# Performance work log

Measured on AMD Instinct MI355X. Metric: run time of the kernel, lower is better.

Reference implementation:

```python
import jax, jax.numpy as jnp
import numpy as np

N_OBJ = 4096     # number of tree nodes (objects)
IN_DIM = 1024    # inputs_dim (visual feature per node)
EMB = 200        # GloVe embed_dim
HID = 1024       # hidden_dim
NCLS = 151       # len(classes)
IN_SIZE = IN_DIM + EMB  # backward direction: inputs_dim + embed_dim


def _linear_params(k, fan_in, fan_out):
    kw, kb = jax.random.split(k)
    s = 1.0 / np.sqrt(fan_in)
    W = jax.random.uniform(kw, (fan_out, fan_in), jnp.float32, -s, s)
    b = jax.random.uniform(kb, (fan_out,), jnp.float32, -s, s)
    return W, b


def setup_inputs() -> dict:
    key = jax.random.key(0)
    ks = jax.random.split(key, 8)
    features = jax.random.normal(ks[0], (N_OBJ, IN_DIM), jnp.float32)
    embed_W = jax.random.normal(ks[1], (NCLS + 1, EMB), jnp.float32)  # row 0 = 'start'
    W_px, b_px = _linear_params(ks[2], IN_SIZE, HID)
    W_ioux, b_ioux = _linear_params(ks[3], IN_SIZE, 3 * HID)
    W_iouh, b_iouh = _linear_params(ks[4], HID, 3 * HID)
    W_fx, b_fx = _linear_params(ks[5], IN_SIZE, HID)
    W_fh, b_fh = _linear_params(ks[6], HID, HID)
    W_out, b_out = _linear_params(ks[7], HID, NCLS)
    # Irregular random tree in preorder: parent step index always < own step index.
    rng = np.random.RandomState(0)
    parent_pos = np.floor(rng.rand(N_OBJ) * np.arange(N_OBJ)).astype(np.int32)
    parent_pos[0] = -1  # root
    proc_order = rng.permutation(N_OBJ).astype(np.int32)  # node index visited at step t
    return dict(features=features, embed_W=embed_W,
                W_px=W_px, b_px=b_px, W_ioux=W_ioux, b_ioux=b_ioux,
                W_iouh=W_iouh, b_iouh=b_iouh, W_fx=W_fx, b_fx=b_fx,
                W_fh=W_fh, b_fh=b_fh, W_out=W_out, b_out=b_out,
                proc_order=jnp.asarray(proc_order), parent_pos=jnp.asarray(parent_pos),
                num_obj=N_OBJ)


def reference(features, embed_W, W_px, b_px, W_ioux, b_ioux, W_iouh, b_iouh,
              W_fx, b_fx, W_fh, b_fh, W_out, b_out, proc_order, parent_pos, num_obj):
    N = features.shape[0]
    H = W_fh.shape[0]

    def step(carry, t):
        h_all, c_all, lab_all = carry  # states/labels indexed by visit step
        pid = parent_pos[t]
        is_root = pid < 0
        pidc = jnp.maximum(pid, 0)
        ph = jnp.where(is_root, 0.0, h_all[pidc])  # parent hidden (root -> zeros)
        pc = jnp.where(is_root, 0.0, c_all[pidc])  # parent cell
        # input embedding: parent's predicted label (+1 for 'start' offset), root uses 'start' (row 0)
        eidx = jnp.where(is_root, 0, lab_all[pidc] + 1)
        feat = jnp.concatenate([features[proc_order[t]], embed_W[eidx]])  # [IN_SIZE]
        # tree-LSTM cell (node_backward)
        projected_x = W_px @ feat + b_px
        iou = W_ioux @ feat + b_ioux + W_iouh @ ph + b_iouh
        i, o, u = jnp.split(iou, 3)
        i = jax.nn.sigmoid(i); o = jax.nn.sigmoid(o); u = jnp.tanh(u)
        f = jax.nn.sigmoid(W_fx @ feat + b_fx + W_fh @ ph + b_fh)
        c = i * u + f * pc
        h = o * jnp.tanh(c) * jax.nn.sigmoid(projected_x)  # highway-style gate
        dist = W_out @ h + b_out  # [NCLS]
        label = (jnp.argmax(dist[1:]) + 1).astype(jnp.int32)  # skip background, eval-mode argmax
        return (h_all.at[t].set(h), c_all.at[t].set(c), lab_all.at[t].set(label)), (dist, label)

    init = (jnp.zeros((N, H), features.dtype),
            jnp.zeros((N, H), features.dtype),
            jnp.zeros((N,), jnp.int32))
    _, (dists, labels) = jax.lax.scan(step, init, jnp.arange(N))
    # scatter back from visit order to node order (out[node] = value at its visit step)
    out_dists = jnp.zeros_like(dists).at[proc_order].set(dists)
    out_commitments = jnp.zeros((N,), jnp.int32).at[proc_order].set(labels)
    return out_dists, out_commitments
```

## Files before the change

kernel.cpp:

```cpp
#include <hip/hip_runtime.h>
#include <hip/hip_bf16.h>
#include <math.h>

#define N_OBJ 4096
#define IN_DIM 1024
#define EMB_D 200
#define HID 1024
#define NCLS 151
#define IN_SZ 1224
#define NEMB 152
#define R5 5120
#define RH 4096
#define MAXLVL 32

typedef __attribute__((ext_vector_type(8))) short bf16x8;
typedef __attribute__((ext_vector_type(4))) float f32x4;

__device__ __forceinline__ float sigf(float x) { return 1.f / (1.f + expf(-x)); }

__device__ __forceinline__ void split2(float x, ushort& hi, ushort& lo) {
    unsigned u = __float_as_uint(x);
    unsigned r = u + 0x7FFFu + ((u >> 16) & 1u);
    hi = (ushort)(r >> 16);
    float rem = x - __uint_as_float(r & 0xFFFF0000u);
    unsigned u2 = __float_as_uint(rem);
    unsigned r2 = u2 + 0x7FFFu + ((u2 >> 16) & 1u);
    lo = (ushort)(r2 >> 16);
}

__device__ __forceinline__ void gload16(const ushort* src, ushort* dst) {
    __builtin_amdgcn_global_load_lds(
        (const __attribute__((address_space(1))) void*)src,
        (__attribute__((address_space(3))) void*)dst, 16, 0, 0);
}

__global__ __launch_bounds__(1024)
void build_levels(const int* __restrict__ parent_pos,
                  int* __restrict__ level_nodes,
                  int* __restrict__ level_start,
                  ushort* __restrict__ zpad)
{
    __shared__ int dep[N_OBJ];
    __shared__ int par[N_OBJ];
    __shared__ int cnt[MAXLVL];
    __shared__ int offs[MAXLVL];
    __shared__ int base[MAXLVL + 1];
    __shared__ int done;
    const int tid = threadIdx.x;

    if (tid < 1024) zpad[tid] = 0;

    for (int t = tid; t < N_OBJ; t += 1024) {
        int p = parent_pos[t];
        par[t] = p;
        dep[t] = (p < 0) ? 0 : -1;
    }
    for (int l = tid; l < MAXLVL; l += 1024) { cnt[l] = 0; offs[l] = 0; }
    __syncthreads();

    for (int it = 0; it < 64; ++it) {
        if (tid == 0) done = 1;
        __syncthreads();
        for (int t = tid; t < N_OBJ; t += 1024) {
            if (dep[t] < 0) {
                int dp = dep[par[t]];
                if (dp >= 0) dep[t] = dp + 1;
                else done = 0;
            }
        }
        __syncthreads();
        int d = done;
        __syncthreads();
        if (d) break;
    }

    for (int t = tid; t < N_OBJ; t += 1024) {
        int d = dep[t];
        if (d < 0 || d >= MAXLVL) d = MAXLVL - 1;
        dep[t] = d;
        atomicAdd(&cnt[d], 1);
    }
    __syncthreads();
    if (tid == 0) {
        base[0] = 0;
        for (int l = 0; l < MAXLVL; ++l) base[l + 1] = base[l] + cnt[l];
    }
    __syncthreads();
    for (int t = tid; t < N_OBJ; t += 1024) {
        int d = dep[t];
        int pos = base[d] + atomicAdd(&offs[d], 1);
        level_nodes[pos] = t;
    }
    for (int l = tid; l <= MAXLVL; l += 1024) level_start[l] = base[l];
}

__global__ __launch_bounds__(256)
void xemb_kernel(const float* __restrict__ embed_W,
                 const float* __restrict__ W_px,
                 const float* __restrict__ W_ioux,
                 const float* __restrict__ W_fx,
                 const float* __restrict__ b_px,
                 const float* __restrict__ b_ioux,
                 const float* __restrict__ b_iouh,
                 const float* __restrict__ b_fx,
                 const float* __restrict__ b_fh,
                 float* __restrict__ Xemb)
{
    __shared__ float e_s[EMB_D];
    const int e = blockIdx.x;
    const int r = blockIdx.y * 256 + threadIdx.x;
    for (int k = threadIdx.x; k < EMB_D; k += 256) e_s[k] = embed_W[(size_t)e * EMB_D + k];
    __syncthreads();

    const float* wrow;
    float bias;
    if (r < HID) {
        wrow = W_px + (size_t)r * IN_SZ;
        bias = b_px[r];
    } else if (r < 4 * HID) {
        wrow = W_ioux + (size_t)(r - HID) * IN_SZ;
        bias = b_ioux[r - HID] + b_iouh[r - HID];
    } else {
        wrow = W_fx + (size_t)(r - 4 * HID) * IN_SZ;
        bias = b_fx[r - 4 * HID] + b_fh[r - 4 * HID];
    }

    float s = bias;
    for (int k = 0; k < EMB_D; ++k) s += wrow[IN_DIM + k] * e_s[k];
    Xemb[(size_t)e * R5 + r] = s;
}

__global__ __launch_bounds__(256)
void convert_wh(const float* __restrict__ W_iouh, const float* __restrict__ W_fh,
                ushort* __restrict__ Whh, ushort* __restrict__ Whl)
{
    const int idx = (blockIdx.x * 256 + threadIdx.x) * 4;
    const int row = idx >> 10, k = idx & 1023;
    const float* src = (row < 3 * HID) ? (W_iouh + (size_t)row * HID + k)
                                       : (W_fh + (size_t)(row - 3 * HID) * HID + k);
    float4 v = *(const float4*)src;
    ushort4 hi, lo;
    split2(v.x, hi.x, lo.x); split2(v.y, hi.y, lo.y);
    split2(v.z, hi.z, lo.z); split2(v.w, hi.w, lo.w);
    *(ushort4*)(Whh + (size_t)row * HID + k) = hi;
    *(ushort4*)(Whl + (size_t)row * HID + k) = lo;
}

__global__ __launch_bounds__(256)
void convert_wx(const float* __restrict__ W_px, const float* __restrict__ W_ioux,
                const float* __restrict__ W_fx,
                ushort* __restrict__ Wxh, ushort* __restrict__ Wxl)
{
    const int idx = (blockIdx.x * 256 + threadIdx.x) * 4;
    const int row = idx >> 10, k = idx & 1023;
    const float* src;
    if (row < HID)          src = W_px   + (size_t)row * IN_SZ + k;
    else if (row < 4 * HID) src = W_ioux + (size_t)(row - HID) * IN_SZ + k;
    else                    src = W_fx   + (size_t)(row - 4 * HID) * IN_SZ + k;
    float4 v = *(const float4*)src;
    ushort4 hi, lo;
    split2(v.x, hi.x, lo.x); split2(v.y, hi.y, lo.y);
    split2(v.z, hi.z, lo.z); split2(v.w, hi.w, lo.w);
    *(ushort4*)(Wxh + (size_t)row * IN_DIM + k) = hi;
    *(ushort4*)(Wxl + (size_t)row * IN_DIM + k) = lo;
}

__global__ __launch_bounds__(256)
void convert_f(const float* __restrict__ features, const int* __restrict__ proc_order,
               ushort* __restrict__ Fh, ushort* __restrict__ Fl)
{
    const int idx = (blockIdx.x * 256 + threadIdx.x) * 4;
    const int t = idx >> 10, k = idx & 1023;
    const float* src = features + (size_t)proc_order[t] * IN_DIM + k;
    float4 v = *(const float4*)src;
    ushort4 hi, lo;
    split2(v.x, hi.x, lo.x); split2(v.y, hi.y, lo.y);
    split2(v.z, hi.z, lo.z); split2(v.w, hi.w, lo.w);
    *(ushort4*)(Fh + (size_t)t * IN_DIM + k) = hi;
    *(ushort4*)(Fl + (size_t)t * IN_DIM + k) = lo;
}

__global__ __launch_bounds__(256, 2)
void xgemm_mfma(const ushort* __restrict__ Fh, const ushort* __restrict__ Fl,
                const ushort* __restrict__ Wxh, const ushort* __restrict__ Wxl,
                float* __restrict__ Hbuf)
{
    const int bid = blockIdx.x;
    const int sup = bid >> 6, within = bid & 63;
    const int bm = (sup & 3) * 8 + (within & 7);
    const int bn = (sup >> 2) * 8 + (within >> 3);

    __shared__ __align__(16) ushort smem[2][4][128 * 32];

    const int tid = threadIdx.x;
    const int lane = tid & 63;
    const int wid = tid >> 6;
    const int wm = wid & 1, wn = wid >> 1;
    const int g = lane >> 4;
    const int lr = lane >> 2, cg4 = lane & 3;

    const ushort* gsrc =
        (wid == 0) ? Fh  + (size_t)(bm * 128) * IN_DIM :
        (wid == 1) ? Fl  + (size_t)(bm * 128) * IN_DIM :
        (wid == 2) ? Wxh + (size_t)(bn * 128) * IN_DIM :
                     Wxl + (size_t)(bn * 128) * IN_DIM;

    f32x4 acc[4][4];
    #pragma unroll
    for (int i = 0; i < 4; ++i)
        #pragma unroll
        for (int j = 0; j < 4; ++j)
            acc[i][j] = (f32x4){0.f, 0.f, 0.f, 0.f};

    #pragma unroll
    for (int i = 0; i < 8; ++i) {
        int row = i * 16 + lr;
        int cs = (cg4 ^ ((row >> 1) & 3)) << 3;
        gload16(gsrc + (size_t)row * IN_DIM + cs, &smem[0][wid][i * 512]);
    }
    __syncthreads();

    int cur = 0;
    for (int kc = 0; kc < IN_DIM / 32; ++kc) {
        if (kc + 1 < IN_DIM / 32) {
            const int kt = (kc + 1) * 32;
            #pragma unroll
            for (int i = 0; i < 8; ++i) {
                int row = i * 16 + lr;
                int cs = (cg4 ^ ((row >> 1) & 3)) << 3;
                gload16(gsrc + (size_t)row * IN_DIM + kt + cs, &smem[cur ^ 1][wid][i * 512]);
            }
        }
        const ushort* Ahb = &smem[cur][0][0];
        const ushort* Alb = &smem[cur][1][0];
        const ushort* Bhb = &smem[cur][2][0];
        const ushort* Blb = &smem[cur][3][0];
        bf16x8 fa[8];
        #pragma unroll
        for (int mi = 0; mi < 4; ++mi) {
            int row = wm * 64 + mi * 16 + (lane & 15);
            int off = row * 32 + ((g ^ ((row >> 1) & 3)) << 3);
            fa[2 * mi]     = *(const bf16x8*)&Ahb[off];
            fa[2 * mi + 1] = *(const bf16x8*)&Alb[off];
        }
        #pragma unroll
        for (int ni = 0; ni < 4; ++ni) {
            int row = wn * 64 + ni * 16 + (lane & 15);
            int off = row * 32 + ((g ^ ((row >> 1) & 3)) << 3);
            bf16x8 fbh = *(const bf16x8*)&Bhb[off];
            bf16x8 fbl = *(const bf16x8*)&Blb[off];
            #pragma unroll
            for (int mi = 0; mi < 4; ++mi) {
                acc[mi][ni] = __builtin_amdgcn_mfma_f32_16x16x32_bf16(fa[2*mi],   fbh, acc[mi][ni], 0, 0, 0);
                acc[mi][ni] = __builtin_amdgcn_mfma_f32_16x16x32_bf16(fa[2*mi],   fbl, acc[mi][ni], 0, 0, 0);
                acc[mi][ni] = __builtin_amdgcn_mfma_f32_16x16x32_bf16(fa[2*mi+1], fbh, acc[mi][ni], 0, 0, 0);
            }
        }
        __syncthreads();
        cur ^= 1;
    }

    float* Cs = (float*)&smem[0][0][0];
    const int t0 = bm * 128, c0 = bn * 128;
    const int r4 = (lane >> 4) * 4;
    #pragma unroll
    for (int p = 0; p < 2; ++p) {
        if (wm == p) {
            #pragma unroll
            for (int mi = 0; mi < 4; ++mi)
                #pragma unroll
                for (int ni = 0; ni < 4; ++ni) {
                    int row = mi * 16 + r4;
                    int col = wn * 64 + ni * 16 + (lane & 15);
                    #pragma unroll
                    for (int r = 0; r < 4; ++r)
                        Cs[(row + r) * 132 + col] = acc[mi][ni][r];
                }
        }
        __syncthreads();
        #pragma unroll
        for (int i = 0; i < 8; ++i) {
            int row = i * 8 + (tid >> 5);
            float4 v = *(const float4*)&Cs[row * 132 + (tid & 31) * 4];
            *(float4*)&Hbuf[(size_t)(t0 + p * 64 + row) * R5 + c0 + (tid & 31) * 4] = v;
        }
        __syncthreads();
    }
}

__device__ __forceinline__ void hgemm_tile(
    int s0, int n, int bm, int bn,
    const int* __restrict__ level_nodes, const int* __restrict__ parent_pos,
    const ushort* __restrict__ hh, const ushort* __restrict__ hl,
    const ushort* __restrict__ Whh, const ushort* __restrict__ Whl,
    const ushort* __restrict__ zpad, float* __restrict__ Hbuf,
    ushort* csm, int* s_node, int* s_par)
{
    const int tid = threadIdx.x;
    const int lane = tid & 63;
    const int wid = tid >> 6;
    const int wm = wid & 1, wn = wid >> 1;
    const int g = lane >> 4;
    const int lr = lane >> 2, cg4 = lane & 3;

    if (tid < 64) {
        int m = bm * 64 + tid;
        if (m < n) {
            int t = level_nodes[s0 + m];
            s_node[tid] = t;
            s_par[tid]  = parent_pos[t];
        } else { s_node[tid] = -1; s_par[tid] = -1; }
    }
    __syncthreads();

    f32x4 acc[2][4];
    #pragma unroll
    for (int i = 0; i < 2; ++i)
        #pragma unroll
        for (int j = 0; j < 4; ++j)
            acc[i][j] = (f32x4){0.f, 0.f, 0.f, 0.f};

    auto stage = [&](int buf, int kt) {
        ushort* base = csm + buf * 12288;
        if (wid < 2) {
            const ushort* hsrc = (wid == 0) ? hh : hl;
            ushort* ld = base + wid * 2048;
            #pragma unroll
            for (int i = 0; i < 4; ++i) {
                int row = i * 16 + lr;
                int cs = (cg4 ^ ((row >> 1) & 3)) << 3;
                int par = s_par[row];
                const ushort* sp = (par >= 0) ? (hsrc + (size_t)par * HID + kt + cs)
                                              : (zpad + cs);
                gload16(sp, ld + i * 512);
            }
        } else {
            const ushort* wsrc = (wid == 2) ? Whh : Whl;
            ushort* ld = base + 4096 + (wid - 2) * 4096;
            #pragma unroll
            for (int i = 0; i < 8; ++i) {
                int row = i * 16 + lr;
                int cs = (cg4 ^ ((row >> 1) & 3)) << 3;
                gload16(wsrc + (size_t)(bn * 128 + row) * HID + kt + cs, ld + i * 512);
            }
        }
    };

    stage(0, 0);
    __syncthreads();
    int cur = 0;
    for (int kc = 0; kc < HID / 32; ++kc) {
        if (kc + 1 < HID / 32) stage(cur ^ 1, (kc + 1) * 32);
        const ushort* base = csm + cur * 12288;
        const ushort* Ahb = base;
        const ushort* Alb = base + 2048;
        const ushort* Bhb = base + 4096;
        const ushort* Blb = base + 8192;
        bf16x8 fa[4];
        #pragma unroll
        for (int mi = 0; mi < 2; ++mi) {
            int row = wm * 32 + mi * 16 + (lane & 15);
            int off = row * 32 + ((g ^ ((row >> 1) & 3)) << 3);
            fa[2 * mi]     = *(const bf16x8*)&Ahb[off];
            fa[2 * mi + 1] = *(const bf16x8*)&Alb[off];
        }
        #pragma unroll
        for (int ni = 0; ni < 4; ++ni) {
            int row = wn * 64 + ni * 16 + (lane & 15);
            int off = row * 32 + ((g ^ ((row >> 1) & 3)) << 3);
            bf16x8 fbh = *(const bf16x8*)&Bhb[off];
            bf16x8 fbl = *(const bf16x8*)&Blb[off];
            #pragma unroll
            for (int mi = 0; mi < 2; ++mi) {
                acc[mi][ni] = __builtin_amdgcn_mfma_f32_16x16x32_bf16(fa[2*mi],   fbh, acc[mi][ni], 0, 0, 0);
                acc[mi][ni] = __builtin_amdgcn_mfma_f32_16x16x32_bf16(fa[2*mi],   fbl, acc[mi][ni], 0, 0, 0);
                acc[mi][ni] = __builtin_amdgcn_mfma_f32_16x16x32_bf16(fa[2*mi+1], fbh, acc[mi][ni], 0, 0, 0);
            }
        }
        __syncthreads();
        cur ^= 1;
    }

    float* Cs = (float*)csm;
    const int r4 = (lane >> 4) * 4;
    #pragma unroll
    for (int mi = 0; mi < 2; ++mi)
        #pragma unroll
        for (int ni = 0; ni < 4; ++ni) {
            int row = wm * 32 + mi * 16 + r4;
            int col = wn * 64 + ni * 16 + (lane & 15);
            #pragma unroll
            for (int r = 0; r < 4; ++r)
                Cs[(row + r) * 132 + col] = acc[mi][ni][r];
        }
    __syncthreads();
    #pragma unroll
    for (int i = 0; i < 8; ++i) {
        int row = i * 8 + (tid >> 5);
        if (bm * 64 + row < n) {
            int t = s_node[row];
            float* dst = Hbuf + (size_t)t * R5 + HID + bn * 128 + (tid & 31) * 4;
            float4 o = *(const float4*)dst;
            const float* cp = &Cs[row * 132 + (tid & 31) * 4];
            o.x += cp[0]; o.y += cp[1]; o.z += cp[2]; o.w += cp[3];
            *(float4*)dst = o;
        }
    }
}

__device__ __forceinline__ void gates_dist_node(
    int t,
    const int* __restrict__ proc_order, const int* __restrict__ parent_pos,
    const float* __restrict__ Hbuf, const float* __restrict__ Xemb,
    const float* __restrict__ W_out, const float* __restrict__ b_out,
    ushort* __restrict__ hh, ushort* __restrict__ hl,
    float* __restrict__ c_all, int* __restrict__ eidx_all, float* __restrict__ out,
    float* hs, float* bv_s, int* bi_s)
{
    const int tid = threadIdx.x;
    const int pid = parent_pos[t];
    const int eidx = (pid < 0) ? 0 : eidx_all[pid];

    const float4* H4 = (const float4*)(Hbuf + (size_t)t * R5);
    const float4* E4 = (const float4*)(Xemb + (size_t)eidx * R5);

    float4 Hpx = H4[tid],        Epx = E4[tid];
    float4 Hi  = H4[256 + tid],  Ei  = E4[256 + tid];
    float4 Ho  = H4[512 + tid],  Eo  = E4[512 + tid];
    float4 Hu  = H4[768 + tid],  Eu  = E4[768 + tid];
    float4 Hf  = H4[1024 + tid], Ef  = E4[1024 + tid];
    float4 PC = (pid < 0) ? make_float4(0.f, 0.f, 0.f, 0.f)
                          : ((const float4*)(c_all + (size_t)pid * HID))[tid];

    float cv[4], hv[4];
#define GATE(CP, IDX) { \
    float pxv = Hpx.CP + Epx.CP; \
    float iv  = Hi.CP + Ei.CP; \
    float ov  = Ho.CP + Eo.CP; \
    float uv  = Hu.CP + Eu.CP; \
    float fv  = Hf.CP + Ef.CP; \
    float ig = sigf(iv), og = sigf(ov), ug = tanhf(uv), fg = sigf(fv); \
    float cc = ig * ug + fg * PC.CP; \
    cv[IDX] = cc; \
    hv[IDX] = og * tanhf(cc) * sigf(pxv); }
    GATE(x, 0) GATE(y, 1) GATE(z, 2) GATE(w, 3)
#undef GATE

    float4 c4 = make_float4(cv[0], cv[1], cv[2], cv[3]);
    float4 h4 = make_float4(hv[0], hv[1], hv[2], hv[3]);
    ((float4*)(c_all + (size_t)t * HID))[tid] = c4;
    ((float4*)hs)[tid] = h4;
    ushort4 shi, slo;
    split2(h4.x, shi.x, slo.x); split2(h4.y, shi.y, slo.y);
    split2(h4.z, shi.z, slo.z); split2(h4.w, shi.w, slo.w);
    *(ushort4*)(hh + (size_t)t * HID + (tid << 2)) = shi;
    *(ushort4*)(hl + (size_t)t * HID + (tid << 2)) = slo;
    __syncthreads();

    const int node = proc_order[t];
    float* dists = out + (size_t)node * NCLS;
    const int wave = tid >> 6, lane = tid & 63;

    float bv = -3.4e38f; int bi = NCLS;
    for (int r = wave; r < NCLS; r += 4) {
        const float* wr = W_out + (size_t)r * HID;
        float s = 0.f;
        #pragma unroll
        for (int q = 0; q < 4; ++q) {
            float4 w4 = *(const float4*)(wr + (lane << 2) + q * 256);
            float4 x4 = *(const float4*)(hs + (lane << 2) + q * 256);
            s += w4.x * x4.x + w4.y * x4.y + w4.z * x4.z + w4.w * x4.w;
        }
        #pragma unroll
        for (int off = 32; off > 0; off >>= 1) s += __shfl_down(s, off, 64);
        if (lane == 0) {
            s += b_out[r];
            dists[r] = s;
            if (r >= 1 && s > bv) { bv = s; bi = r; }
        }
    }
    if (lane == 0) { bv_s[wave] = bv; bi_s[wave] = bi; }
    __syncthreads();
    if (tid == 0) {
        float v = bv_s[0]; int b = bi_s[0];
        for (int w = 1; w < 4; ++w)
            if (bv_s[w] > v || (bv_s[w] == v && bi_s[w] < b)) { v = bv_s[w]; b = bi_s[w]; }
        eidx_all[t] = b + 1;
        out[(size_t)N_OBJ * NCLS + node] = (float)b;
    }
    __syncthreads();
}

__global__ __launch_bounds__(256, 2)
void hgemm_lvl(int lvl, const int* __restrict__ level_start,
               const int* __restrict__ level_nodes, const int* __restrict__ parent_pos,
               const ushort* __restrict__ hh, const ushort* __restrict__ hl,
               const ushort* __restrict__ Whh, const ushort* __restrict__ Whl,
               const ushort* __restrict__ zpad, float* __restrict__ Hbuf)
{
    __shared__ __align__(16) ushort csm[24576];
    __shared__ int s_node[64], s_par[64];
    const int s0 = level_start[lvl];
    const int n  = level_start[lvl + 1] - s0;
    const int bm = blockIdx.y;
    if (bm * 64 >= n) return;
    hgemm_tile(s0, n, bm, blockIdx.x, level_nodes, parent_pos,
               hh, hl, Whh, Whl, zpad, Hbuf, csm, s_node, s_par);
}

__global__ __launch_bounds__(256, 2)
void gates_lvl(int lvl, const int* __restrict__ level_start,
               const int* __restrict__ level_nodes, const int* __restrict__ proc_order,
               const int* __restrict__ parent_pos,
               const float* __restrict__ Hbuf, const float* __restrict__ Xemb,
               const float* __restrict__ W_out, const float* __restrict__ b_out,
               ushort* __restrict__ hh, ushort* __restrict__ hl,
               float* __restrict__ c_all, int* __restrict__ eidx_all,
               float* __restrict__ out)
{
    __shared__ __align__(16) float hs[HID];
    __shared__ float bv_s[4];
    __shared__ int bi_s[4];
    const int s0 = level_start[lvl];
    const int n  = level_start[lvl + 1] - s0;
    for (int slot = blockIdx.x; slot < n; slot += gridDim.x) {
        int t = level_nodes[s0 + slot];
        gates_dist_node(t, proc_order, parent_pos, Hbuf, Xemb, W_out, b_out,
                        hh, hl, c_all, eidx_all, out, hs, bv_s, bi_s);
    }
}

extern "C" void kernel_launch(void* const* d_in, const int* in_sizes, int n_in,
                              void* d_out, int out_size, void* d_ws, size_t ws_size,
                              hipStream_t stream)
{
    const float* features = (const float*)d_in[0];
    const float* embed_W  = (const float*)d_in[1];
    const float* W_px     = (const float*)d_in[2];
    const float* b_px     = (const float*)d_in[3];
    const float* W_ioux   = (const float*)d_in[4];
    const float* b_ioux   = (const float*)d_in[5];
    const float* W_iouh   = (const float*)d_in[6];
    const float* b_iouh   = (const float*)d_in[7];
    const float* W_fx     = (const float*)d_in[8];
    const float* b_fx     = (const float*)d_in[9];
    const float* W_fh     = (const float*)d_in[10];
    const float* b_fh     = (const float*)d_in[11];
    const float* W_out    = (const float*)d_in[12];
    const float* b_out    = (const float*)d_in[13];
    const int* proc_order = (const int*)d_in[14];
    const int* parent_pos = (const int*)d_in[15];
    float* out = (float*)d_out;

    float* Hbuf  = (float*)d_ws;
    float* c_all = Hbuf + (size_t)N_OBJ * R5;
    float* Xemb  = c_all + (size_t)N_OBJ * HID;
    ushort* Whh = (ushort*)(Xemb + (size_t)NEMB * R5);
    ushort* Whl = Whh + (size_t)RH * HID;
    ushort* Wxh = Whl + (size_t)RH * HID;
    ushort* Wxl = Wxh + (size_t)R5 * IN_DIM;
    ushort* Fh  = Wxl + (size_t)R5 * IN_DIM;
    ushort* Fl  = Fh + (size_t)N_OBJ * IN_DIM;
    ushort* hh  = Fl + (size_t)N_OBJ * IN_DIM;
    ushort* hl  = hh + (size_t)N_OBJ * HID;
    ushort* zpad = hl + (size_t)N_OBJ * HID;
    int* eidx_all    = (int*)(zpad + 1024);
    int* level_nodes = eidx_all + N_OBJ;
    int* level_start = level_nodes + N_OBJ;

    build_levels<<<1, 1024, 0, stream>>>(parent_pos, level_nodes, level_start, zpad);
    xemb_kernel<<<dim3(NEMB, R5 / 256), 256, 0, stream>>>(
        embed_W, W_px, W_ioux, W_fx, b_px, b_ioux, b_iouh, b_fx, b_fh, Xemb);
    convert_wh<<<RH * HID / 1024, 256, 0, stream>>>(W_iouh, W_fh, Whh, Whl);
    convert_wx<<<R5 * IN_DIM / 1024, 256, 0, stream>>>(W_px, W_ioux, W_fx, Wxh, Wxl);
    convert_f<<<N_OBJ * IN_DIM / 1024, 256, 0, stream>>>(features, proc_order, Fh, Fl);

    xgemm_mfma<<<(N_OBJ / 128) * (R5 / 128), 256, 0, stream>>>(Fh, Fl, Wxh, Wxl, Hbuf);

    for (int l = 0; l < MAXLVL; ++l) {
        if (l > 0)
            hgemm_lvl<<<dim3(32, 64), 256, 0, stream>>>(
                l, level_start, level_nodes, parent_pos,
                hh, hl, Whh, Whl, zpad, Hbuf);
        gates_lvl<<<512, 256, 0, stream>>>(
            l, level_start, level_nodes, proc_order, parent_pos,
            Hbuf, Xemb, W_out, b_out, hh, hl, c_all, eidx_all, out);
    }
}
```

Measured before the change: 1.322 ms.

## Move embedding projection and output classifier onto split-bf16 MFMA GEMMs

Replaces the scalar per-row embedding projection kernel with an MFMA GEMM over padded hi/lo bf16 copies of the embedding table and embedding weight columns, with biases precomputed into a vector. The per-level gates kernel now processes 32 nodes per block and computes the output classifier as a split-bf16 MFMA tile GEMM against a pre-converted W_out, replacing the per-node dot-product reduction. This removes redundant re-reading of W_out per node and scalar FMA work, at the cost of extra conversion kernels, workspace, and a three-term bf16 split approximation for the logits, which could flip argmax ties.

```diff
diff --git a/kernel.cpp b/kernel.cpp
--- a/kernel.cpp
+++ b/kernel.cpp
@@ -7,8 +7,10 @@
 #define EMB_D 200
 #define HID 1024
 #define NCLS 151
+#define NCPAD 160
 #define IN_SZ 1224
 #define NEMB 152
+#define KE 224
 #define R5 5120
 #define RH 4096
 #define MAXLVL 32
@@ -92,42 +94,6 @@
         level_nodes[pos] = t;
     }
     for (int l = tid; l <= MAXLVL; l += 1024) level_start[l] = base[l];
-}
-
-__global__ __launch_bounds__(256)
-void xemb_kernel(const float* __restrict__ embed_W,
-                 const float* __restrict__ W_px,
-                 const float* __restrict__ W_ioux,
-                 const float* __restrict__ W_fx,
-                 const float* __restrict__ b_px,
-                 const float* __restrict__ b_ioux,
-                 const float* __restrict__ b_iouh,
-                 const float* __restrict__ b_fx,
-                 const float* __restrict__ b_fh,
-                 float* __restrict__ Xemb)
-{
-    __shared__ float e_s[EMB_D];
-    const int e = blockIdx.x;
-    const int r = blockIdx.y * 256 + threadIdx.x;
-    for (int k = threadIdx.x; k < EMB_D; k += 256) e_s[k] = embed_W[(size_t)e * EMB_D + k];
-    __syncthreads();
-
-    const float* wrow;
-    float bias;
-    if (r < HID) {
-        wrow = W_px + (size_t)r * IN_SZ;
-        bias = b_px[r];
-    } else if (r < 4 * HID) {
-        wrow = W_ioux + (size_t)(r - HID) * IN_SZ;
-        bias = b_ioux[r - HID] + b_iouh[r - HID];
-    } else {
-        wrow = W_fx + (size_t)(r - 4 * HID) * IN_SZ;
-        bias = b_fx[r - 4 * HID] + b_fh[r - 4 * HID];
-    }
-
-    float s = bias;
-    for (int k = 0; k < EMB_D; ++k) s += wrow[IN_DIM + k] * e_s[k];
-    Xemb[(size_t)e * R5 + r] = s;
 }
 
 __global__ __launch_bounds__(256)
@@ -180,15 +146,80 @@
     *(ushort4*)(Fl + (size_t)t * IN_DIM + k) = lo;
 }
 
+__global__ __launch_bounds__(256)
+void convert_wout(const float* __restrict__ W_out,
+                  ushort* __restrict__ Woh, ushort* __restrict__ Wol)
+{
+    const int idx = (blockIdx.x * 256 + threadIdx.x) * 4;
+    const int row = idx >> 10, k = idx & 1023;
+    float4 v = make_float4(0.f, 0.f, 0.f, 0.f);
+    if (row < NCLS) v = *(const float4*)(W_out + (size_t)row * HID + k);
+    ushort4 hi, lo;
+    split2(v.x, hi.x, lo.x); split2(v.y, hi.y, lo.y);
+    split2(v.z, hi.z, lo.z); split2(v.w, hi.w, lo.w);
+    *(ushort4*)(Woh + (size_t)row * HID + k) = hi;
+    *(ushort4*)(Wol + (size_t)row * HID + k) = lo;
+}
+
+__global__ __launch_bounds__(256)
+void convert_e(const float* __restrict__ embed_W,
+               ushort* __restrict__ Eh, ushort* __restrict__ El)
+{
+    const int idx = (blockIdx.x * 256 + threadIdx.x) * 4;
+    const int row = idx / KE, c = idx % KE;
+    float4 v = make_float4(0.f, 0.f, 0.f, 0.f);
+    if (row < NEMB && c < EMB_D) v = *(const float4*)(embed_W + (size_t)row * EMB_D + c);
+    ushort4 hi, lo;
+    split2(v.x, hi.x, lo.x); split2(v.y, hi.y, lo.y);
+    split2(v.z, hi.z, lo.z); split2(v.w, hi.w, lo.w);
+    *(ushort4*)(Eh + (size_t)row * KE + c) = hi;
+    *(ushort4*)(El + (size_t)row * KE + c) = lo;
+}
+
+__global__ __launch_bounds__(256)
+void convert_wemb(const float* __restrict__ W_px, const float* __restrict__ W_ioux,
+                  const float* __restrict__ W_fx,
+                  ushort* __restrict__ Wembh, ushort* __restrict__ Wembl)
+{
+    const int idx = (blockIdx.x * 256 + threadIdx.x) * 4;
+    const int row = idx / KE, c = idx % KE;
+    float4 v = make_float4(0.f, 0.f, 0.f, 0.f);
+    if (c < EMB_D) {
+        const float* src;
+        if (row < HID)          src = W_px   + (size_t)row * IN_SZ + IN_DIM + c;
+        else if (row < 4 * HID) src = W_ioux + (size_t)(row - HID) * IN_SZ + IN_DIM + c;
+        else                    src = W_fx   + (size_t)(row - 4 * HID) * IN_SZ + IN_DIM + c;
+        v = *(const float4*)src;
+    }
+    ushort4 hi, lo;
+    split2(v.x, hi.x, lo.x); split2(v.y, hi.y, lo.y);
+    split2(v.z, hi.z, lo.z); split2(v.w, hi.w, lo.w);
+    *(ushort4*)(Wembh + (size_t)row * KE + c) = hi;
+    *(ushort4*)(Wembl + (size_t)row * KE + c) = lo;
+}
+
+__global__ __launch_bounds__(256)
+void bias_kernel(const float* __restrict__ b_px,
+                 const float* __restrict__ b_ioux, const float* __restrict__ b_iouh,
+                 const float* __restrict__ b_fx, const float* __restrict__ b_fh,
+                 float* __restrict__ biasv)
+{
+    const int r = blockIdx.x * 256 + threadIdx.x;
+    float b;
+    if (r < HID)          b = b_px[r];
+    else if (r < 4 * HID) b = b_ioux[r - HID] + b_iouh[r - HID];
+    else                  b = b_fx[r - 4 * HID] + b_fh[r - 4 * HID];
+    biasv[r] = b;
+}
+
 __global__ __launch_bounds__(256, 2)
-void xgemm_mfma(const ushort* __restrict__ Fh, const ushort* __restrict__ Fl,
-                const ushort* __restrict__ Wxh, const ushort* __restrict__ Wxl,
-                float* __restrict__ Hbuf)
-{
-    const int bid = blockIdx.x;
-    const int sup = bid >> 6, within = bid & 63;
-    const int bm = (sup & 3) * 8 + (within & 7);
-    const int bn = (sup >> 2) * 8 + (within >> 3);
+void xemb_mfma(const ushort* __restrict__ Eh, const ushort* __restrict__ El,
+               const ushort* __restrict__ Wembh, const ushort* __restrict__ Wembl,
+               const float* __restrict__ biasv,
+               float* __restrict__ Xemb)
+{
+    const int bm = blockIdx.y;
+    const int bn = blockIdx.x;
 
     __shared__ __align__(16) ushort smem[2][4][128 * 32];
 
@@ -200,10 +231,10 @@
     const int lr = lane >> 2, cg4 = lane & 3;
 
     const ushort* gsrc =
-        (wid == 0) ? Fh  + (size_t)(bm * 128) * IN_DIM :
-        (wid == 1) ? Fl  + (size_t)(bm * 128) * IN_DIM :
-        (wid == 2) ? Wxh + (size_t)(bn * 128) * IN_DIM :
-                     Wxl + (size_t)(bn * 128) * IN_DIM;
+        (wid == 0) ? Eh    + (size_t)(bm * 128) * KE :
+        (wid == 1) ? El    + (size_t)(bm * 128) * KE :
+        (wid == 2) ? Wembh + (size_t)(bn * 128) * KE :
+                     Wembl + (size_t)(bn * 128) * KE;
 
     f32x4 acc[4][4];
     #pragma unroll
@@ -216,19 +247,19 @@
     for (int i = 0; i < 8; ++i) {
         int row = i * 16 + lr;
         int cs = (cg4 ^ ((row >> 1) & 3)) << 3;
-        gload16(gsrc + (size_t)row * IN_DIM + cs, &smem[0][wid][i * 512]);
+        gload16(gsrc + (size_t)row * KE + cs, &smem[0][wid][i * 512]);
     }
     __syncthreads();
 
     int cur = 0;
-    for (int kc = 0; kc < IN_DIM / 32; ++kc) {
-        if (kc + 1 < IN_DIM / 32) {
+    for (int kc = 0; kc < KE / 32; ++kc) {
+        if (kc + 1 < KE / 32) {
             const int kt = (kc + 1) * 32;
             #pragma unroll
             for (int i = 0; i < 8; ++i) {
                 int row = i * 16 + lr;
                 int cs = (cg4 ^ ((row >> 1) & 3)) << 3;
-                gload16(gsrc + (size_t)row * IN_DIM + kt + cs, &smem[cur ^ 1][wid][i * 512]);
+                gload16(gsrc + (size_t)row * KE + kt + cs, &smem[cur ^ 1][wid][i * 512]);
             }
         }
         const ushort* Ahb = &smem[cur][0][0];
@@ -261,8 +292,9 @@
     }
 
     float* Cs = (float*)&smem[0][0][0];
-    const int t0 = bm * 128, c0 = bn * 128;
+    const int c0 = bn * 128;
     const int r4 = (lane >> 4) * 4;
+    float4 b4 = *(const float4*)&biasv[c0 + (tid & 31) * 4];
     #pragma unroll
     for (int p = 0; p < 2; ++p) {
         if (wm == p) {
@@ -281,6 +313,118 @@
         #pragma unroll
         for (int i = 0; i < 8; ++i) {
             int row = i * 8 + (tid >> 5);
+            int erow = bm * 128 + p * 64 + row;
+            if (erow < NEMB) {
+                float4 v = *(const float4*)&Cs[row * 132 + (tid & 31) * 4];
+                v.x += b4.x; v.y += b4.y; v.z += b4.z; v.w += b4.w;
+                *(float4*)&Xemb[(size_t)erow * R5 + c0 + (tid & 31) * 4] = v;
+            }
+        }
+        __syncthreads();
+    }
+}
+
+__global__ __launch_bounds__(256, 2)
+void xgemm_mfma(const ushort* __restrict__ Fh, const ushort* __restrict__ Fl,
+                const ushort* __restrict__ Wxh, const ushort* __restrict__ Wxl,
+                float* __restrict__ Hbuf)
+{
+    const int bid = blockIdx.x;
+    const int sup = bid >> 6, within = bid & 63;
+    const int bm = (sup & 3) * 8 + (within & 7);
+    const int bn = (sup >> 2) * 8 + (within >> 3);
+
+    __shared__ __align__(16) ushort smem[2][4][128 * 32];
+
+    const int tid = threadIdx.x;
+    const int lane = tid & 63;
+    const int wid = tid >> 6;
+    const int wm = wid & 1, wn = wid >> 1;
+    const int g = lane >> 4;
+    const int lr = lane >> 2, cg4 = lane & 3;
+
+    const ushort* gsrc =
+        (wid == 0) ? Fh  + (size_t)(bm * 128) * IN_DIM :
+        (wid == 1) ? Fl  + (size_t)(bm * 128) * IN_DIM :
+        (wid == 2) ? Wxh + (size_t)(bn * 128) * IN_DIM :
+                     Wxl + (size_t)(bn * 128) * IN_DIM;
+
+    f32x4 acc[4][4];
+    #pragma unroll
+    for (int i = 0; i < 4; ++i)
+        #pragma unroll
+        for (int j = 0; j < 4; ++j)
+            acc[i][j] = (f32x4){0.f, 0.f, 0.f, 0.f};
+
+    #pragma unroll
+    for (int i = 0; i < 8; ++i) {
+        int row = i * 16 + lr;
+        int cs = (cg4 ^ ((row >> 1) & 3)) << 3;
+        gload16(gsrc + (size_t)row * IN_DIM + cs, &smem[0][wid][i * 512]);
+    }
+    __syncthreads();
+
+    int cur = 0;
+    for (int kc = 0; kc < IN_DIM / 32; ++kc) {
+        if (kc + 1 < IN_DIM / 32) {
+            const int kt = (kc + 1) * 32;
+            #pragma unroll
+            for (int i = 0; i < 8; ++i) {
+                int row = i * 16 + lr;
+                int cs = (cg4 ^ ((row >> 1) & 3)) << 3;
+                gload16(gsrc + (size_t)row * IN_DIM + kt + cs, &smem[cur ^ 1][wid][i * 512]);
+            }
+        }
+        const ushort* Ahb = &smem[cur][0][0];
+        const ushort* Alb = &smem[cur][1][0];
+        const ushort* Bhb = &smem[cur][2][0];
+        const ushort* Blb = &smem[cur][3][0];
+        bf16x8 fa[8];
+        #pragma unroll
+        for (int mi = 0; mi < 4; ++mi) {
+            int row = wm * 64 + mi * 16 + (lane & 15);
+            int off = row * 32 + ((g ^ ((row >> 1) & 3)) << 3);
+            fa[2 * mi]     = *(const bf16x8*)&Ahb[off];
+            fa[2 * mi + 1] = *(const bf16x8*)&Alb[off];
+        }
+        #pragma unroll
+        for (int ni = 0; ni < 4; ++ni) {
+            int row = wn * 64 + ni * 16 + (lane & 15);
+            int off = row * 32 + ((g ^ ((row >> 1) & 3)) << 3);
+            bf16x8 fbh = *(const bf16x8*)&Bhb[off];
+            bf16x8 fbl = *(const bf16x8*)&Blb[off];
+            #pragma unroll
+            for (int mi = 0; mi < 4; ++mi) {
+                acc[mi][ni] = __builtin_amdgcn_mfma_f32_16x16x32_bf16(fa[2*mi],   fbh, acc[mi][ni], 0, 0, 0);
+                acc[mi][ni] = __builtin_amdgcn_mfma_f32_16x16x32_bf16(fa[2*mi],   fbl, acc[mi][ni], 0, 0, 0);
+                acc[mi][ni] = __builtin_amdgcn_mfma_f32_16x16x32_bf16(fa[2*mi+1], fbh, acc[mi][ni], 0, 0, 0);
+            }
+        }
+        __syncthreads();
+        cur ^= 1;
+    }
+
+    float* Cs = (float*)&smem[0][0][0];
+    const int t0 = bm * 128, c0 = bn * 128;
+    const int r4 = (lane >> 4) * 4;
+    #pragma unroll
+    for (int p = 0; p < 2; ++p) {
+        if (wm == p) {
+            #pragma unroll
+            for (int mi = 0; mi < 4; ++mi)
+                #pragma unroll
+                for (int ni = 0; ni < 4; ++ni) {
+                    int row = mi * 16 + r4;
+                    int col = wn * 64 + ni * 16 + (lane & 15);
+                    #pragma unroll
+                    for (int r = 0; r < 4; ++r)
+                        Cs[(row + r) * 132 + col] = acc[mi][ni][r];
+                }
+        }
+        __syncthreads();
+        #pragma unroll
+        for (int i = 0; i < 8; ++i) {
+            int row = i * 8 + (tid >> 5);
             float4 v = *(const float4*)&Cs[row * 132 + (tid & 31) * 4];
             *(float4*)&Hbuf[(size_t)(t0 + p * 64 + row) * R5 + c0 + (tid & 31) * 4] = v;
         }
@@ -408,89 +552,6 @@
     }
 }
 
-__device__ __forceinline__ void gates_dist_node(
-    int t,
-    const int* __restrict__ proc_order, const int* __restrict__ parent_pos,
-    const float* __restrict__ Hbuf, const float* __restrict__ Xemb,
-    const float* __restrict__ W_out, const float* __restrict__ b_out,
-    ushort* __restrict__ hh, ushort* __restrict__ hl,
-    float* __restrict__ c_all, int* __restrict__ eidx_all, float* __restrict__ out,
-    float* hs, float* bv_s, int* bi_s)
-{
-    const int tid = threadIdx.x;
-    const int pid = parent_pos[t];
-    const int eidx = (pid < 0) ? 0 : eidx_all[pid];
-
-    const float4* H4 = (const float4*)(Hbuf + (size_t)t * R5);
-    const float4* E4 = (const float4*)(Xemb + (size_t)eidx * R5);
-
-    float4 Hpx = H4[tid],        Epx = E4[tid];
-    float4 Hi  = H4[256 + tid],  Ei  = E4[256 + tid];
-    float4 Ho  = H4[512 + tid],  Eo  = E4[512 + tid];
-    float4 Hu  = H4[768 + tid],  Eu  = E4[768 + tid];
-    float4 Hf  = H4[1024 + tid], Ef  = E4[1024 + tid];
-    float4 PC = (pid < 0) ? make_float4(0.f, 0.f, 0.f, 0.f)
-                          : ((const float4*)(c_all + (size_t)pid * HID))[tid];
-
-    float cv[4], hv[4];
-#define GATE(CP, IDX) { \
-    float pxv = Hpx.CP + Epx.CP; \
-    float iv  = Hi.CP + Ei.CP; \
-    float ov  = Ho.CP + Eo.CP; \
-    float uv  = Hu.CP + Eu.CP; \
-    float fv  = Hf.CP + Ef.CP; \
-    float ig = sigf(iv), og = sigf(ov), ug = tanhf(uv), fg = sigf(fv); \
-    float cc = ig * ug + fg * PC.CP; \
-    cv[IDX] = cc; \
-    hv[IDX] = og * tanhf(cc) * sigf(pxv); }
-    GATE(x, 0) GATE(y, 1) GATE(z, 2) GATE(w, 3)
-#undef GATE
-
-    float4 c4 = make_float4(cv[0], cv[1], cv[2], cv[3]);
-    float4 h4 = make_float4(hv[0], hv[1], hv[2], hv[3]);
-    ((float4*)(c_all + (size_t)t * HID))[tid] = c4;
-    ((float4*)hs)[tid] = h4;
-    ushort4 shi, slo;
-    split2(h4.x, shi.x, slo.x); split2(h4.y, shi.y, slo.y);
-    split2(h4.z, shi.z, slo.z); split2(h4.w, shi.w, slo.w);
-    *(ushort4*)(hh + (size_t)t * HID + (tid << 2)) = shi;
-    *(ushort4*)(hl + (size_t)t * HID + (tid << 2)) = slo;
-    __syncthreads();
-
-    const int node = proc_order[t];
-    float* dists = out + (size_t)node * NCLS;
-    const int wave = tid >> 6, lane = tid & 63;
-
-    float bv = -3.4e38f; int bi = NCLS;
-    for (int r = wave; r < NCLS; r += 4) {
-        const float* wr = W_out + (size_t)r * HID;
-        float s = 0.f;
-        #pragma unroll
-        for (int q = 0; q < 4; ++q) {
-            float4 w4 = *(const float4*)(wr + (lane << 2) + q * 256);
-            float4 x4 = *(const float4*)(hs + (lane << 2) + q * 256);
-            s += w4.x * x4.x + w4.y * x4.y + w4.z * x4.z + w4.w * x4.w;
-        }
-        #pragma unroll
-        for (int off = 32; off > 0; off >>= 1) s += __shfl_down(s, off, 64);
-        if (lane == 0) {
-            s += b_out[r];
-            dists[r] = s;
-            if (r >= 1 && s > bv) { bv = s; bi = r; }
-        }
-    }
-    if (lane == 0) { bv_s[wave] = bv; bi_s[wave] = bi; }
-    __syncthreads();
-    if (tid == 0) {
-        float v = bv_s[0]; int b = bi_s[0];
-        for (int w = 1; w < 4; ++w)
-            if (bv_s[w] > v || (bv_s[w] == v && bi_s[w] < b)) { v = bv_s[w]; b = bi_s[w]; }
-        eidx_all[t] = b + 1;
-        out[(size_t)N_OBJ * NCLS + node] = (float)b;
-    }
-    __syncthreads();
-}
-
 __global__ __launch_bounds__(256, 2)
 void hgemm_lvl(int lvl, const int* __restrict__ level_start,
                const int* __restrict__ level_nodes, const int* __restrict__ parent_pos,
@@ -509,24 +570,182 @@
 }
 
 __global__ __launch_bounds__(256, 2)
-void gates_lvl(int lvl, const int* __restrict__ level_start,
-               const int* __restrict__ level_nodes, const int* __restrict__ proc_order,
-               const int* __restrict__ parent_pos,
-               const float* __restrict__ Hbuf, const float* __restrict__ Xemb,
-               const float* __restrict__ W_out, const float* __restrict__ b_out,
-               ushort* __restrict__ hh, ushort* __restrict__ hl,
-               float* __restrict__ c_all, int* __restrict__ eidx_all,
-               float* __restrict__ out)
-{
-    __shared__ __align__(16) float hs[HID];
-    __shared__ float bv_s[4];
-    __shared__ int bi_s[4];
+void gates_dist(int lvl,
+                const int* __restrict__ level_start,
+                const int* __restrict__ level_nodes,
+                const int* __restrict__ proc_order,
+                const int* __restrict__ parent_pos,
+                const float* __restrict__ Hbuf,
+                const float* __restrict__ Xemb,
+                const ushort* __restrict__ Woh, const ushort* __restrict__ Wol,
+                const float* __restrict__ b_out,
+                const ushort* __restrict__ zpad,
+                ushort* __restrict__ hh, ushort* __restrict__ hl,
+                float* __restrict__ c_all,
+                int* __restrict__ eidx_all,
+                float* __restrict__ out)
+{
     const int s0 = level_start[lvl];
     const int n  = level_start[lvl + 1] - s0;
-    for (int slot = blockIdx.x; slot < n; slot += gridDim.x) {
-        int t = level_nodes[s0 + slot];
-        gates_dist_node(t, proc_order, parent_pos, Hbuf, Xemb, W_out, b_out,
-                        hh, hl, c_all, eidx_all, out, hs, bv_s, bi_s);
+    const int bm = blockIdx.x;
+    if (bm * 32 >= n) return;
+    const int tid = threadIdx.x;
+    const int lane = tid & 63;
+    const int wid = tid >> 6;
+    const int wm = wid & 1, wn = wid >> 1;
+
+    __shared__ __align__(16) ushort smem[384 * 72];
+    ushort* Ah = smem;
+    ushort* Al = smem + 32 * 72;
+    ushort* Bh = smem + 64 * 72;
+    ushort* Bl = smem + 224 * 72;
+    __shared__ int s_node[32];
+
+    if (tid < 32) {
+        int m = bm * 32 + tid;
+        s_node[tid] = (m < n) ? level_nodes[s0 + m] : -1;
+    }
+    __syncthreads();
+
+    const int m = tid >> 3, sub = tid & 7;
+    const int t = s_node[m];
+    if (t >= 0) {
+        const int pid = parent_pos[t];
+        const int eidx = (pid < 0) ? 0 : eidx_all[pid];
+        const float4* H4 = (const float4*)(Hbuf + (size_t)t * R5);
+        const float4* E4 = (const float4*)(Xemb + (size_t)eidx * R5);
+        const float4* PC4 = (pid < 0) ? nullptr : (const float4*)(c_all + (size_t)pid * HID);
+        float4* C4 = (float4*)(c_all + (size_t)t * HID);
+        ushort* hhp = hh + (size_t)t * HID;
+        ushort* hlp = hl + (size_t)t * HID;
+        for (int i = 0; i < 32; ++i) {
+            const int j = i * 8 + sub;
+            float4 Hpx = H4[j],        Epx = E4[j];
+            float4 Hi  = H4[256 + j],  Ei  = E4[256 + j];
+            float4 Ho  = H4[512 + j],  Eo  = E4[512 + j];
+            float4 Hu  = H4[768 + j],  Eu  = E4[768 + j];
+            float4 Hf  = H4[1024 + j], Ef  = E4[1024 + j];
+            float4 PC = PC4 ? PC4[j] : make_float4(0.f, 0.f, 0.f, 0.f);
+
+            float cv[4], hv[4];
+#define GATE(CP, IDX) { \
+            float pxv = Hpx.CP + Epx.CP; \
+            float iv  = Hi.CP + Ei.CP; \
+            float ov  = Ho.CP + Eo.CP; \
+            float uv  = Hu.CP + Eu.CP; \
+            float fv  = Hf.CP + Ef.CP; \
+            float ig = sigf(iv), og = sigf(ov), ug = tanhf(uv), fg = sigf(fv); \
+            float cc = ig * ug + fg * PC.CP; \
+            cv[IDX] = cc; \
+            hv[IDX] = og * tanhf(cc) * sigf(pxv); }
+            GATE(x, 0) GATE(y, 1) GATE(z, 2) GATE(w, 3)
+#undef GATE
+
+            C4[j] = make_float4(cv[0], cv[1], cv[2], cv[3]);
+            ushort4 shi, slo;
+            split2(hv[0], shi.x, slo.x); split2(hv[1], shi.y, slo.y);
+            split2(hv[2], shi.z, slo.z); split2(hv[3], shi.w, slo.w);
+            *(ushort4*)(hhp + j * 4) = shi;
+            *(ushort4*)(hlp + j * 4) = slo;
+        }
+    }
+    __syncthreads();
+
+    const int arow = tid >> 3, apc = (tid & 7) * 8;
+    const int ta = s_node[arow];
+    const ushort* gAh = (ta >= 0 ? hh + (size_t)ta * HID : zpad) + apc;
+    const ushort* gAl = (ta >= 0 ? hl + (size_t)ta * HID : zpad) + apc;
+
+    f32x4 acc[5];
+    #pragma unroll
+    for (int f = 0; f < 5; ++f) acc[f] = (f32x4){0.f, 0.f, 0.f, 0.f};
+
+    uint4 rA0, rA1, rB0[5], rB1[5];
+    rA0 = *(const uint4*)gAh;
+    rA1 = *(const uint4*)gAl;
+    #pragma unroll
+    for (int j = 0; j < 5; ++j) {
+        int i = tid + j * 256;
+        int brow = i >> 3, bpc = (i & 7) * 8;
+        rB0[j] = *(const uint4*)(Woh + (size_t)brow * HID + bpc);
+        rB1[j] = *(const uint4*)(Wol + (size_t)brow * HID + bpc);
+    }
+
+    for (int kc = 0; kc < HID / 64; ++kc) {
+        __syncthreads();
+        *(uint4*)&Ah[arow * 72 + apc] = rA0;
+        *(uint4*)&Al[arow * 72 + apc] = rA1;
+        #pragma unroll
+        for (int j = 0; j < 5; ++j) {
+            int i = tid + j * 256;
+            int brow = i >> 3, bpc = (i & 7) * 8;
+            *(uint4*)&Bh[brow * 72 + bpc] = rB0[j];
+            *(uint4*)&Bl[brow * 72 + bpc] = rB1[j];
+        }
+        __syncthreads();
+        if (kc + 1 < HID / 64) {
+            const int kt = (kc + 1) * 64;
+            rA0 = *(const uint4*)(gAh + kt);
+            rA1 = *(const uint4*)(gAl + kt);
+            #pragma unroll
+            for (int j = 0; j < 5; ++j) {
+                int i = tid + j * 256;
+                int brow = i >> 3, bpc = (i & 7) * 8;
+                rB0[j] = *(const uint4*)(Woh + (size_t)brow * HID + kt + bpc);
+                rB1[j] = *(const uint4*)(Wol + (size_t)brow * HID + kt + bpc);
+            }
+        }
+        const int g = lane >> 4;
+        #pragma unroll
+        for (int s = 0; s < 2; ++s) {
+            int ao = (wm * 16 + (lane & 15)) * 72 + s * 32 + g * 8;
+            bf16x8 fah = *(const bf16x8*)&Ah[ao];
+            bf16x8 fal = *(const bf16x8*)&Al[ao];
+            #pragma unroll
+            for (int f = 0; f < 5; ++f) {
+                int bo = (wn * 80 + f * 16 + (lane & 15)) * 72 + s * 32 + g * 8;
+                bf16x8 fbh = *(const bf16x8*)&Bh[bo];
+                bf16x8 fbl = *(const bf16x8*)&Bl[bo];
+                acc[f] = __builtin_amdgcn_mfma_f32_16x16x32_bf16(fah, fbh, acc[f], 0, 0, 0);
+                acc[f] = __builtin_amdgcn_mfma_f32_16x16x32_bf16(fah, fbl, acc[f], 0, 0, 0);
+                acc[f] = __builtin_amdgcn_mfma_f32_16x16x32_bf16(fal, fbh, acc[f], 0, 0, 0);
+            }
+        }
+    }
+
+    __syncthreads();
+    float* ds = (float*)smem;
+    const int r4 = (lane >> 4) * 4;
+    #pragma unroll
+    for (int f = 0; f < 5; ++f) {
+        const int col = wn * 80 + f * 16 + (lane & 15);
+        const int row = wm * 16 + r4;
+        #pragma unroll
+        for (int r = 0; r < 4; ++r)
+            ds[(row + r) * 172 + col] = acc[f][r];
+    }
+    __syncthreads();
+
+    float bv = -3.4e38f; int bc = NCLS;
+    if (bm * 32 + m < n) {
+        const int tt = s_node[m];
+        const int node = proc_order[tt];
+        float* drow = out + (size_t)node * NCLS;
+        for (int c = sub; c < NCLS; c += 8) {
+            float v = ds[m * 172 + c] + b_out[c];
+            drow[c] = v;
+            if (c >= 1 && (v > bv || (v == bv && c < bc))) { bv = v; bc = c; }
+        }
+        #pragma unroll
+        for (int off = 4; off > 0; off >>= 1) {
+            float ov = __shfl_down(bv, off, 64);
+            int   oc = __shfl_down(bc, off, 64);
+            if (ov > bv || (ov == bv && oc < bc)) { bv = ov; bc = oc; }
+        }
+        if (sub == 0) {
+            eidx_all[tt] = bc + 1;
+            out[(size_t)N_OBJ * NCLS + node] = (float)bc;
+        }
     }
 }
 
@@ -555,7 +774,8 @@
     float* Hbuf  = (float*)d_ws;
     float* c_all = Hbuf + (size_t)N_OBJ * R5;
     float* Xemb  = c_all + (size_t)N_OBJ * HID;
-    ushort* Whh = (ushort*)(Xemb + (size_t)NEMB * R5);
+    float* biasv = Xemb + (size_t)NEMB * R5;
+    ushort* Whh = (ushort*)(biasv + R5);
     ushort* Whl = Whh + (size_t)RH * HID;
     ushort* Wxh = Whl + (size_t)RH * HID;
     ushort* Wxl = Wxh + (size_t)R5 * IN_DIM;
@@ -563,18 +783,27 @@
     ushort* Fl  = Fh + (size_t)N_OBJ * IN_DIM;
     ushort* hh  = Fl + (size_t)N_OBJ * IN_DIM;
     ushort* hl  = hh + (size_t)N_OBJ * HID;
-    ushort* zpad = hl + (size_t)N_OBJ * HID;
+    ushort* Woh = hl + (size_t)N_OBJ * HID;
+    ushort* Wol = Woh + (size_t)NCPAD * HID;
+    ushort* Eh  = Wol + (size_t)NCPAD * HID;
+    ushort* El  = Eh + (size_t)256 * KE;
+    ushort* Wembh = El + (size_t)256 * KE;
+    ushort* Wembl = Wembh + (size_t)R5 * KE;
+    ushort* zpad = Wembl + (size_t)R5 * KE;
     int* eidx_all    = (int*)(zpad + 1024);
     int* level_nodes = eidx_all + N_OBJ;
     int* level_start = level_nodes + N_OBJ;
 
     build_levels<<<1, 1024, 0, stream>>>(parent_pos, level_nodes, level_start, zpad);
-    xemb_kernel<<<dim3(NEMB, R5 / 256), 256, 0, stream>>>(
-        embed_W, W_px, W_ioux, W_fx, b_px, b_ioux, b_iouh, b_fx, b_fh, Xemb);
     convert_wh<<<RH * HID / 1024, 256, 0, stream>>>(W_iouh, W_fh, Whh, Whl);
     convert_wx<<<R5 * IN_DIM / 1024, 256, 0, stream>>>(W_px, W_ioux, W_fx, Wxh, Wxl);
     convert_f<<<N_OBJ * IN_DIM / 1024, 256, 0, stream>>>(features, proc_order, Fh, Fl);
-
+    convert_wout<<<NCPAD * HID / 1024, 256, 0, stream>>>(W_out, Woh, Wol);
+    convert_e<<<256 * KE / 1024, 256, 0, stream>>>(embed_W, Eh, El);
+    convert_wemb<<<R5 * KE / 1024, 256, 0, stream>>>(W_px, W_ioux, W_fx, Wembh, Wembl);
+    bias_kernel<<<R5 / 256, 256, 0, stream>>>(b_px, b_ioux, b_iouh, b_fx, b_fh, biasv);
+
+    xemb_mfma<<<dim3(R5 / 128, 2), 256, 0, stream>>>(Eh, El, Wembh, Wembl, biasv, Xemb);
     xgemm_mfma<<<(N_OBJ / 128) * (R5 / 128), 256, 0, stream>>>(Fh, Fl, Wxh, Wxl, Hbuf);
 
     for (int l = 0; l < MAXLVL; ++l) {
@@ -582,8 +811,8 @@
             hgemm_lvl<<<dim3(32, 64), 256, 0, stream>>>(
                 l, level_start, level_nodes, parent_pos,
                 hh, hl, Whh, Whl, zpad, Hbuf);
-        gates_lvl<<<512, 256, 0, stream>>>(
+        gates_dist<<<N_OBJ / 32, 256, 0, stream>>>(
             l, level_start, level_nodes, proc_order, parent_pos,
-            Hbuf, Xemb, W_out, b_out, hh, hl, c_all, eidx_all, out);
-    }
-}
+            Hbuf, Xemb, Woh, Wol, b_out, zpad, hh, hl, c_all, eidx_all, out);
+    }
+}
```

Measured after the change: 2.442 ms. 84.7% more time.
